# Optimization experiments

Hardware: AMD Instinct MI355X
Metric: run time of the kernel (lower is better)

The kernel has to match this reference:

```python
import jax, jax.numpy as jnp
import numpy as np

B, N, D_MODEL = 2, 1536, 512
MIN_WL, MAX_WL, BASE = 3.7, 20.0, 20.0
COORD_SCALE = 8.0  # Angstrom-ish spread so pair distances span the wavelength band
EPS = 1e-6


def setup_inputs() -> dict:
    key = jax.random.key(0)
    k1, _ = jax.random.split(key)
    coords = jax.random.normal(k1, (B, N, 3), dtype=jnp.float32) * COORD_SCALE
    key_padding_mask = jnp.zeros((B, N), dtype=bool)  # True = padded
    K = D_MODEL // 2
    # buffer from __init__: min_wl + (max_wl-min_wl)*(logspace(0,1,K,base)-1)/(base-1)
    wavelengths = MIN_WL + (MAX_WL - MIN_WL) * (jnp.logspace(0.0, 1.0, K, base=BASE) - 1.0) / (BASE - 1.0)
    wavenumbers = (2.0 * jnp.pi / wavelengths).astype(jnp.float32)
    return {"coords": coords, "key_padding_mask": key_padding_mask, "wavenumbers": wavenumbers}


def reference(coords, key_padding_mask, wavenumbers):
    # coords: [B,N,3]; key_padding_mask: [B,N] (True = pad); wavenumbers: [K]
    b, n, _ = coords.shape
    diff = coords[:, :, None, :] - coords[:, None, :, :]          # [B,N,N,3]
    r = jnp.sqrt(jnp.sum(diff * diff, axis=-1) + 1e-12)            # [B,N,N]
    # valid sources: not padded and not the point itself (Green's fn singular at r=0)
    valid = (~key_padding_mask)[:, None, :] & (~jnp.eye(n, dtype=bool))[None]
    amp = jnp.where(valid, 1.0 / (4.0 * jnp.pi * jnp.maximum(r, EPS)), 0.0)  # [B,N,N]

    # scan over wavenumbers so we never materialize a [B,N,N,K] tensor
    def step(_, k):
        phase = k * r                                              # [B,N,N]
        re = jnp.sum(jnp.cos(phase) * amp, axis=-1)                # [B,N]
        im = jnp.sum(jnp.sin(phase) * amp, axis=-1)                # [B,N]
        return None, (re, im)

    _, (re, im) = jax.lax.scan(step, None, wavenumbers)            # each [K,B,N]
    wf = jnp.stack([re, im], axis=-1)                              # [K,B,N,2]
    wf = jnp.moveaxis(wf, 0, 2)                                    # [B,N,K,2]
    return wf.reshape(b, n, -1)                                    # [B,N,d_model]
```

## Files before the change

kernel.cpp:

```cpp
#include <hip/hip_runtime.h>
#include <math.h>


#define N_FIXED  1536
#define K_FIXED  256
#define QBINS    256
#define QG       260
#define ROWS     4
#define RSTRIDE  272
#define NTHREADS 512
#define FPSCALE  4194304.0f

__global__ __launch_bounds__(256) void wf_direct_kernel(
    const float* __restrict__ coords, const unsigned char* __restrict__ mask,
    const float* __restrict__ wavenumbers, float* __restrict__ out, int N, int K)
{
    __shared__ float2 pairs[N_FIXED];
    const int row = blockIdx.x;
    const int b   = row / N;
    const int i   = row - b * N;
    const int t   = threadIdx.x;
    const float* crow = coords + (size_t)b * N * 3;
    const float xi = crow[i*3+0], yi = crow[i*3+1], zi = crow[i*3+2];
    const unsigned char* mrow = mask + (size_t)b * N;
    for (int j = t; j < N; j += blockDim.x) {
        float dx = crow[j*3+0]-xi, dy = crow[j*3+1]-yi, dz = crow[j*3+2]-zi;
        float d2 = fmaf(dx,dx, fmaf(dy,dy, fmaf(dz,dz, 1e-12f)));
        float r  = sqrtf(d2);
        float amp = 0.07957747154594767f / fmaxf(r, 1e-6f);
        if (j == i || mrow[j]) amp = 0.0f;
        pairs[j] = make_float2(r, amp);
    }
    __syncthreads();
    const int k = t;
    const float f = wavenumbers[k] * 0.15915494309189535f;
    float re = 0.0f, im = 0.0f;
    #pragma unroll 4
    for (int j = 0; j < N; ++j) {
        float2 p = pairs[j];
        float x  = __builtin_amdgcn_fractf(p.x * f);
        float c  = __builtin_amdgcn_cosf(x);
        float s  = __builtin_amdgcn_sinf(x);
        re = fmaf(c, p.y, re);
        im = fmaf(s, p.y, im);
    }
    float2* orow = (float2*)out + (size_t)row * K;
    orow[k] = make_float2(re, im);
}

__global__ __launch_bounds__(NTHREADS) void wf_fused_kernel(
    const float* __restrict__ coords, const unsigned char* __restrict__ mask,
    const float* __restrict__ wavenumbers, float* __restrict__ out, int N)
{
    __shared__ int    hist[ROWS * RSTRIDE];
    __shared__ float  red[8];
    __shared__ float2 merge[ROWS * K_FIXED];

    const int i0 = blockIdx.x * ROWS;
    const int b  = i0 / N;
    const int t  = threadIdx.x;

    const float* crow = coords + (size_t)b * N * 3;
    const unsigned char* mrow = mask + (size_t)b * N;

    float m = 0.0f;
    #pragma unroll
    for (int s = 0; s < N_FIXED / NTHREADS; ++s) {
        const int p = t + NTHREADS * s;
        float x = crow[3*p], y = crow[3*p+1], z = crow[3*p+2];
        m = fmaxf(m, fmaf(x,x, fmaf(y,y, z*z)));
    }
    #pragma unroll
    for (int off = 32; off >= 1; off >>= 1)
        m = fmaxf(m, __shfl_down(m, off, 64));
    if ((t & 63) == 0) red[t >> 6] = m;
    for (int a = t; a < ROWS * RSTRIDE; a += NTHREADS) hist[a] = 0;
    __syncthreads();
    float mm = red[0];
    #pragma unroll
    for (int w = 1; w < 8; ++w) mm = fmaxf(mm, red[w]);
    const float rmax = 2.0005f * sqrtf(mm) + 1e-3f;
    const float h    = rmax / (float)QBINS;
    const float inv_h = 1.0f / h;

    const int il0 = i0 - b * N;
    float cx[ROWS], cy[ROWS], cz[ROWS];
    #pragma unroll
    for (int r = 0; r < ROWS; ++r) {
        cx[r] = crow[3*(il0+r)];
        cy[r] = crow[3*(il0+r)+1];
        cz[r] = crow[3*(il0+r)+2];
    }

    #pragma unroll
    for (int s = 0; s < N_FIXED / NTHREADS; ++s) {
        const int j = t + NTHREADS * s;
        const float xj = crow[3*j], yj = crow[3*j+1], zj = crow[3*j+2];
        const bool masked = (mrow[j] != 0);
        #pragma unroll
        for (int r = 0; r < ROWS; ++r) {
            float dx = xj - cx[r];
            float dy = yj - cy[r];
            float dz = zj - cz[r];
            float d2 = fmaf(dx,dx, fmaf(dy,dy, fmaf(dz,dz, 1e-12f)));
            float rsq = __builtin_amdgcn_rsqf(d2);
            float amp = 0.07957747154594767f * rsq;
            if (j == il0 + r || masked) amp = 0.0f;

            float u  = d2 * rsq * inv_h;
            float qf = floorf(u);
            int   q0 = (int)qf;
            float tt = u - qf;
            float as6 = amp * (FPSCALE * (1.0f/6.0f));
            float as2 = amp * (FPSCALE * 0.5f);
            float tm1 = tt + 1.0f, t1 = tt - 1.0f, t2 = tt - 2.0f;
            float p  = tt  * t1;
            float qq = tm1 * t2;
            int w0 = (int)(-(p  * t2)  * as6);
            int w1 = (int)( (qq * t1)  * as2);
            int w2 = (int)(-(qq * tt)  * as2);
            int w3 = (int)( (p  * tm1) * as6);
            int* hb = &hist[r * RSTRIDE + q0];
            atomicAdd(hb + 0, w0);
            atomicAdd(hb + 1, w1);
            atomicAdd(hb + 2, w2);
            atomicAdd(hb + 3, w3);
        }
    }
    __syncthreads();

    float* hf = (float*)hist;
    const float invS = 1.0f / FPSCALE;
    for (int a = t; a < ROWS * RSTRIDE; a += NTHREADS)
        hf[a] = (float)hist[a] * invS;
    __syncthreads();

    const int team = t >> 8;
    const int c    = t & 255;
    const int gbeg = team ? 33 : 0;
    const int gend = team ? 65 : 33;
    const int qs   = gbeg * 4;

    const float xrev = wavenumbers[c] * 0.15915494309189535f * h;
    const float k2   = 2.0f * __builtin_amdgcn_cosf(__builtin_amdgcn_fractf(xrev));
    const float aarg = __builtin_amdgcn_fractf((float)(qs - 1) * xrev);
    const float barg = __builtin_amdgcn_fractf((float)qs * xrev);
    float ca = __builtin_amdgcn_cosf(aarg), sa = __builtin_amdgcn_sinf(aarg);
    float cb = __builtin_amdgcn_cosf(barg), sb = __builtin_amdgcn_sinf(barg);

    float are[ROWS], aim[ROWS];
    #pragma unroll
    for (int r = 0; r < ROWS; ++r) { are[r] = 0.0f; aim[r] = 0.0f; }

    #pragma unroll 2
    for (int g = gbeg; g < gend; ++g) {
        const int q0 = g * 4;
        const float4 h0 = *(const float4*)&hf[0 * RSTRIDE + q0];
        const float4 h1 = *(const float4*)&hf[1 * RSTRIDE + q0];
        const float4 h2 = *(const float4*)&hf[2 * RSTRIDE + q0];
        const float4 h3 = *(const float4*)&hf[3 * RSTRIDE + q0];
        const float r0[4] = {h0.x, h0.y, h0.z, h0.w};
        const float r1[4] = {h1.x, h1.y, h1.z, h1.w};
        const float r2[4] = {h2.x, h2.y, h2.z, h2.w};
        const float r3[4] = {h3.x, h3.y, h3.z, h3.w};
        #pragma unroll
        for (int d = 0; d < 4; ++d) {
            are[0] = fmaf(r0[d], ca, are[0]); aim[0] = fmaf(r0[d], sa, aim[0]);
            are[1] = fmaf(r1[d], ca, are[1]); aim[1] = fmaf(r1[d], sa, aim[1]);
            are[2] = fmaf(r2[d], ca, are[2]); aim[2] = fmaf(r2[d], sa, aim[2]);
            are[3] = fmaf(r3[d], ca, are[3]); aim[3] = fmaf(r3[d], sa, aim[3]);
            const float cn = fmaf(k2, cb, -ca);
            const float s2 = fmaf(k2, sb, -sa);
            ca = cb; cb = cn;
            sa = sb; sb = s2;
        }
    }

    if (team == 1) {
        #pragma unroll
        for (int r = 0; r < ROWS; ++r)
            merge[r * K_FIXED + c] = make_float2(are[r], aim[r]);
    }
    __syncthreads();
    if (team == 0) {
        #pragma unroll
        for (int r = 0; r < ROWS; ++r) {
            const float2 p = merge[r * K_FIXED + c];
            ((float2*)out)[(size_t)(i0 + r) * K_FIXED + c] =
                make_float2(are[r] + p.x, aim[r] + p.y);
        }
    }
}

extern "C" void kernel_launch(void* const* d_in, const int* in_sizes, int n_in,
                              void* d_out, int out_size, void* d_ws, size_t ws_size,
                              hipStream_t stream) {
    const float* coords          = (const float*)d_in[0];
    const unsigned char* mask    = (const unsigned char*)d_in[1];
    const float* wavenumbers     = (const float*)d_in[2];
    float* out                   = (float*)d_out;

    const int K  = in_sizes[2];
    const int BN = in_sizes[0] / 3;
    const int N  = N_FIXED;

    if (K != K_FIXED || BN % N != 0 || (N % ROWS) != 0 ||
        (N % NTHREADS) != 0) {
        wf_direct_kernel<<<BN, K, 0, stream>>>(coords, mask, wavenumbers, out, N, K);
        return;
    }

    wf_fused_kernel<<<BN / ROWS, NTHREADS, 0, stream>>>(coords, mask,
                                                        wavenumbers, out, N);
}
```

Before: 75.37 us.

## Split histogram and Fourier sum into bf16 MFMA GEMM kernel

Splits the fused kernel into two. The first kernel builds per-row radial histograms and writes them to workspace as bf16, and it also writes a bf16 cos/sin table sampled at the histogram nodes. A second kernel then computes the wavenumber transform as a GEMM using 16x16x32 bf16 MFMA instructions, replacing the per-thread Chebyshev-recurrence FMA loop. This trades scalar FMA work for matrix-core throughput, at the cost of an extra launch, a global round-trip for the histograms, and reduced precision from bf16 inputs.

```diff
diff --git a/kernel.cpp b/kernel.cpp
--- a/kernel.cpp
+++ b/kernel.cpp
@@ -1,4 +1,5 @@
 #include <hip/hip_runtime.h>
+#include <hip/hip_bf16.h>
 #include <math.h>
 
 
@@ -6,10 +7,13 @@
 #define K_FIXED  256
 #define QBINS    256
 #define QG       260
+#define KDIM     288
 #define ROWS     4
-#define RSTRIDE  272
 #define NTHREADS 512
 #define FPSCALE  4194304.0f
+
+typedef __attribute__((ext_vector_type(8))) short bf16x8;
+typedef __attribute__((ext_vector_type(4))) float f32x4;
 
 __global__ __launch_bounds__(256) void wf_direct_kernel(
     const float* __restrict__ coords, const unsigned char* __restrict__ mask,
@@ -48,33 +52,30 @@
     orow[k] = make_float2(re, im);
 }
 
-__global__ __launch_bounds__(NTHREADS) void wf_fused_kernel(
+__global__ __launch_bounds__(NTHREADS) void wf_hist_kernel(
     const float* __restrict__ coords, const unsigned char* __restrict__ mask,
-    const float* __restrict__ wavenumbers, float* __restrict__ out, int N)
+    const float* __restrict__ wavenumbers,
+    __hip_bfloat16* __restrict__ Wt,
+    __hip_bfloat16* __restrict__ Hb,
+    int n_pts, int N)
 {
-    __shared__ int    hist[ROWS * RSTRIDE];
-    __shared__ float  red[8];
-    __shared__ float2 merge[ROWS * K_FIXED];
+    __shared__ int   hist[ROWS * KDIM];
+    __shared__ float red[8];
 
     const int i0 = blockIdx.x * ROWS;
     const int b  = i0 / N;
     const int t  = threadIdx.x;
 
-    const float* crow = coords + (size_t)b * N * 3;
-    const unsigned char* mrow = mask + (size_t)b * N;
-
     float m = 0.0f;
-    #pragma unroll
-    for (int s = 0; s < N_FIXED / NTHREADS; ++s) {
-        const int p = t + NTHREADS * s;
-        float x = crow[3*p], y = crow[3*p+1], z = crow[3*p+2];
+    for (int p = t; p < n_pts; p += NTHREADS) {
+        float x = coords[3*p], y = coords[3*p+1], z = coords[3*p+2];
         m = fmaxf(m, fmaf(x,x, fmaf(y,y, z*z)));
     }
     #pragma unroll
     for (int off = 32; off >= 1; off >>= 1)
         m = fmaxf(m, __shfl_down(m, off, 64));
     if ((t & 63) == 0) red[t >> 6] = m;
-    for (int a = t; a < ROWS * RSTRIDE; a += NTHREADS) hist[a] = 0;
+    for (int a = t; a < ROWS * KDIM; a += NTHREADS) hist[a] = 0;
     __syncthreads();
     float mm = red[0];
     #pragma unroll
@@ -83,6 +84,20 @@
     const float h    = rmax / (float)QBINS;
     const float inv_h = 1.0f / h;
 
+    if (blockIdx.x < 2 * K_FIXED && t < KDIM) {
+        float v = 0.0f;
+        if (t < QG) {
+            const float rnode = ((float)t - 1.0f) * h;
+            const float arg = __builtin_amdgcn_fractf(
+                wavenumbers[blockIdx.x >> 1] * 0.15915494309189535f * rnode);
+            v = (blockIdx.x & 1) ? __builtin_amdgcn_sinf(arg)
+                                 : __builtin_amdgcn_cosf(arg);
+        }
+        Wt[(size_t)blockIdx.x * KDIM + t] = __float2bfloat16(v);
+    }
+
+    const float* crow = coords + (size_t)b * N * 3;
+    const unsigned char* mrow = mask + (size_t)b * N;
     const int il0 = i0 - b * N;
     float cx[ROWS], cy[ROWS], cz[ROWS];
     #pragma unroll
@@ -120,7 +135,7 @@
             int w1 = (int)( (qq * t1)  * as2);
             int w2 = (int)(-(qq * tt)  * as2);
             int w3 = (int)( (p  * tm1) * as6);
-            int* hb = &hist[r * RSTRIDE + q0];
+            int* hb = &hist[r * KDIM + q0];
             atomicAdd(hb + 0, w0);
             atomicAdd(hb + 1, w1);
             atomicAdd(hb + 2, w2);
@@ -129,67 +144,43 @@
     }
     __syncthreads();
 
-    float* hf = (float*)hist;
+    __hip_bfloat16* Hrow = Hb + (size_t)i0 * KDIM;
     const float invS = 1.0f / FPSCALE;
-    for (int a = t; a < ROWS * RSTRIDE; a += NTHREADS)
-        hf[a] = (float)hist[a] * invS;
-    __syncthreads();
-
-    const int team = t >> 8;
-    const int c    = t & 255;
-    const int gbeg = team ? 33 : 0;
-    const int gend = team ? 65 : 33;
-    const int qs   = gbeg * 4;
-
-    const float xrev = wavenumbers[c] * 0.15915494309189535f * h;
-    const float k2   = 2.0f * __builtin_amdgcn_cosf(__builtin_amdgcn_fractf(xrev));
-    const float aarg = __builtin_amdgcn_fractf((float)(qs - 1) * xrev);
-    const float barg = __builtin_amdgcn_fractf((float)qs * xrev);
-    float ca = __builtin_amdgcn_cosf(aarg), sa = __builtin_amdgcn_sinf(aarg);
-    float cb = __builtin_amdgcn_cosf(barg), sb = __builtin_amdgcn_sinf(barg);
-
-    float are[ROWS], aim[ROWS];
-    #pragma unroll
-    for (int r = 0; r < ROWS; ++r) { are[r] = 0.0f; aim[r] = 0.0f; }
-
-    #pragma unroll 2
-    for (int g = gbeg; g < gend; ++g) {
-        const int q0 = g * 4;
-        const float4 h0 = *(const float4*)&hf[0 * RSTRIDE + q0];
-        const float4 h1 = *(const float4*)&hf[1 * RSTRIDE + q0];
-        const float4 h2 = *(const float4*)&hf[2 * RSTRIDE + q0];
-        const float4 h3 = *(const float4*)&hf[3 * RSTRIDE + q0];
-        const float r0[4] = {h0.x, h0.y, h0.z, h0.w};
-        const float r1[4] = {h1.x, h1.y, h1.z, h1.w};
-        const float r2[4] = {h2.x, h2.y, h2.z, h2.w};
-        const float r3[4] = {h3.x, h3.y, h3.z, h3.w};
-        #pragma unroll
-        for (int d = 0; d < 4; ++d) {
-            are[0] = fmaf(r0[d], ca, are[0]); aim[0] = fmaf(r0[d], sa, aim[0]);
-            are[1] = fmaf(r1[d], ca, are[1]); aim[1] = fmaf(r1[d], sa, aim[1]);
-            are[2] = fmaf(r2[d], ca, are[2]); aim[2] = fmaf(r2[d], sa, aim[2]);
-            are[3] = fmaf(r3[d], ca, are[3]); aim[3] = fmaf(r3[d], sa, aim[3]);
-            const float cn = fmaf(k2, cb, -ca);
-            const float s2 = fmaf(k2, sb, -sa);
-            ca = cb; cb = cn;
-            sa = sb; sb = s2;
-        }
-    }
-
-    if (team == 1) {
-        #pragma unroll
-        for (int r = 0; r < ROWS; ++r)
-            merge[r * K_FIXED + c] = make_float2(are[r], aim[r]);
-    }
-    __syncthreads();
-    if (team == 0) {
-        #pragma unroll
-        for (int r = 0; r < ROWS; ++r) {
-            const float2 p = merge[r * K_FIXED + c];
-            ((float2*)out)[(size_t)(i0 + r) * K_FIXED + c] =
-                make_float2(are[r] + p.x, aim[r] + p.y);
-        }
-    }
+    for (int a = t; a < ROWS * KDIM; a += NTHREADS)
+        Hrow[a] = __float2bfloat16((float)hist[a] * invS);
+}
+
+__global__ __launch_bounds__(256) void wf_gemm_kernel(
+    const __hip_bfloat16* __restrict__ Hb,
+    const __hip_bfloat16* __restrict__ Wt,
+    float* __restrict__ out)
+{
+    const int wave = threadIdx.x >> 6;
+    const int lane = threadIdx.x & 63;
+    const int tile = blockIdx.x * 4 + wave;
+    const int mt   = tile >> 5;
+    const int nt   = tile & 31;
+    const int m0   = mt * 16, n0 = nt * 16;
+    const int quad = lane >> 4, idx = lane & 15;
+
+    const short* Arow = (const short*)Hb + (size_t)(m0 + idx) * KDIM + quad * 8;
+    const short* Brow = (const short*)Wt + (size_t)(n0 + idx) * KDIM + quad * 8;
+
+    bf16x8 a[9], bfr[9];
+    #pragma unroll
+    for (int kk = 0; kk < 9; ++kk) {
+        a[kk]   = *(const bf16x8*)(Arow + kk * 32);
+        bfr[kk] = *(const bf16x8*)(Brow + kk * 32);
+    }
+    f32x4 acc = {0.0f, 0.0f, 0.0f, 0.0f};
+    #pragma unroll
+    for (int kk = 0; kk < 9; ++kk)
+        acc = __builtin_amdgcn_mfma_f32_16x16x32_bf16(a[kk], bfr[kk], acc, 0, 0, 0);
+
+    float* orow = out + (size_t)(m0 + quad * 4) * (2 * K_FIXED) + n0 + idx;
+    #pragma unroll
+    for (int r = 0; r < 4; ++r)
+        orow[(size_t)r * (2 * K_FIXED)] = acc[r];
 }
 
 extern "C" void kernel_launch(void* const* d_in, const int* in_sizes, int n_in,
@@ -204,12 +195,21 @@
     const int BN = in_sizes[0] / 3;
     const int N  = N_FIXED;
 
+    const size_t Wt_bytes = (size_t)(2 * K_FIXED) * KDIM * sizeof(__hip_bfloat16);
+    const size_t need     = Wt_bytes + (size_t)BN * KDIM * sizeof(__hip_bfloat16);
+
     if (K != K_FIXED || BN % N != 0 || (N % ROWS) != 0 ||
-        (N % NTHREADS) != 0) {
+        (N % NTHREADS) != 0 || (BN % 16) != 0 ||
+        (BN / ROWS) < 2 * K_FIXED || ws_size < need) {
         wf_direct_kernel<<<BN, K, 0, stream>>>(coords, mask, wavenumbers, out, N, K);
         return;
     }
 
-    wf_fused_kernel<<<BN / ROWS, NTHREADS, 0, stream>>>(coords, mask,
-                                                        wavenumbers, out, N);
-}
+    __hip_bfloat16* Wt = (__hip_bfloat16*)d_ws;
+    __hip_bfloat16* Hb = Wt + (size_t)(2 * K_FIXED) * KDIM;
+
+    wf_hist_kernel<<<BN / ROWS, NTHREADS, 0, stream>>>(coords, mask,
+                                                       wavenumbers, Wt, Hb, BN, N);
+    const int tiles = (BN / 16) * (2 * K_FIXED / 16);
+    wf_gemm_kernel<<<tiles / 4, 256, 0, stream>>>(Hb, Wt, out);
+}
```

Result: no change. 76.15 us (+1.0%).
